# Kernel tuning notes

Hardware: AMD Instinct MI355X
Metric: run time of the kernel (lower is better)

Reference implementation:

```python
import jax, jax.numpy as jnp
import numpy as np

H = W = 2048
P = 50000  # number of peaks
BACKGROUND = 0.1


def setup_inputs() -> dict:
    key = jax.random.key(0)
    k1, k2, k3, k4 = jax.random.split(key, 4)
    # coordinate meshes, X varies along columns, Y along rows (as in np.meshgrid)
    X, Y = jnp.meshgrid(jnp.arange(W, dtype=jnp.float32), jnp.arange(H, dtype=jnp.float32))
    margin = 32.0
    pos_x = jax.random.uniform(k1, (P,), jnp.float32, margin, W - margin - 1)
    pos_y = jax.random.uniform(k2, (P,), jnp.float32, margin, H - margin - 1)
    height = jax.random.uniform(k3, (P,), jnp.float32, 0.5, 2.0)
    width = jax.random.uniform(k4, (P,), jnp.float32, 2.0, 4.0)
    return {"X": X, "Y": Y, "pos_x": pos_x, "pos_y": pos_y, "height": height, "width": width}


def _gaussian(x, y, pos_x, pos_y, height, width):
    # isotropic Gaussian peak (concrete model_fn)
    r2 = (x - pos_x) ** 2 + (y - pos_y) ** 2
    return height * jnp.exp(-r2 / (2.0 * width ** 2))


def reference(X, Y, pos_x, pos_y, height, width):
    # window size from max width (static shape choice, computed concretely)
    width_max = float(jnp.max(width))
    window_size = int(5 * width_max)
    if window_size % 2 == 0:
        window_size += 1
    half = window_size // 2

    wr = jnp.arange(-half, half + 1, dtype=jnp.int32)
    window_X, window_Y = jnp.meshgrid(wr, wr)  # (ws, ws)
    window_coords = jnp.stack([window_X.ravel(), window_Y.ravel()], axis=-1)  # (ws*ws, 2) as (x, y)

    x_idx = jnp.round(pos_x - X[0, 0]).astype(jnp.int32)
    y_idx = jnp.round(pos_y - Y[0, 0]).astype(jnp.int32)
    peak_coords = jnp.stack([x_idx, y_idx], axis=-1)  # (P, 2)
    global_coords = peak_coords[:, None, :] + window_coords[None, :, :]  # (P, ws*ws, 2)

    # evaluate peak centered at 0 on the local window: (P, ws, ws)
    local_peaks = _gaussian(
        window_X[None, :, :].astype(X.dtype),
        window_Y[None, :, :].astype(X.dtype),
        0.0, 0.0,
        height[:, None, None], width[:, None, None],
    )
    local_flat = local_peaks.reshape(pos_x.shape[0], -1)  # (P, ws*ws)

    total = jnp.zeros_like(X) + BACKGROUND
    total = total.at[global_coords[:, :, 1], global_coords[:, :, 0]].add(local_flat)
    return total
```

## Files before the change

kernel.cpp:

```cpp
#include <hip/hip_runtime.h>


#define IMG_W 2048
#define IMG_H 2048
#define CELL_SHIFT 4
#define CELLS_X 128
#define NCELL (CELLS_X * CELLS_X)
#define CAP 20
#define REG 64
#define CH 32
#define CH_PAD 40
#define CANDMAX 256

typedef _Float16 half8 __attribute__((ext_vector_type(8)));
typedef float floatx4 __attribute__((ext_vector_type(4)));

__global__ void k_bin(const float* __restrict__ px, const float* __restrict__ py,
                      const float* __restrict__ ht, const float* __restrict__ wd,
                      int P, int* __restrict__ counts, unsigned int* __restrict__ wmax,
                      float4* __restrict__ bins) {
    int i = blockIdx.x * blockDim.x + threadIdx.x;
    bool live = (i < P);
    float w = live ? wd[i] : 0.0f;
    float wr = w;
    for (int m = 32; m >= 1; m >>= 1)
        wr = fmaxf(wr, __shfl_xor(wr, m));
    if ((threadIdx.x & 63) == 0)
        atomicMax(wmax, __float_as_uint(wr));
    if (!live) return;
    float cxf = rintf(px[i]);
    float cyf = rintf(py[i]);
    int cell = (((int)cyf) >> CELL_SHIFT) * CELLS_X + (((int)cxf) >> CELL_SHIFT);
    int slot = atomicAdd(&counts[cell], 1);
    if (slot < CAP)
        bins[(size_t)cell * CAP + slot] = make_float4(cxf, cyf, ht[i], -0.5f / (w * w));
}

__global__ __launch_bounds__(512) void k_render(
    const int* __restrict__ counts, const float4* __restrict__ bins,
    const unsigned int* __restrict__ wmax, float* __restrict__ out)
{
    __shared__ _Float16 Afb[2][REG * CH_PAD];
    __shared__ _Float16 Bfb[2][REG * CH_PAD];
    __shared__ float4 cand[CANDMAX];
    __shared__ int ncand_sh;

    int flat = threadIdx.x;
    int wave = flat >> 6;
    int lane = flat & 63;

    float wm = __uint_as_float(*wmax);
    int wsz = (int)(5.0 * (double)wm);
    if ((wsz & 1) == 0) wsz++;
    int half = wsz >> 1;
    float halff = (float)half;

    int RX0 = blockIdx.x * REG;
    int RY0 = blockIdx.y * REG;

    if (flat == 0) ncand_sh = 0;
    __syncthreads();

    int cx0 = max(0, (RX0 - half) >> CELL_SHIFT);
    int cx1 = min(CELLS_X - 1, (RX0 + REG - 1 + half) >> CELL_SHIFT);
    int cy0 = max(0, (RY0 - half) >> CELL_SHIFT);
    int cy1 = min(CELLS_X - 1, (RY0 + REG - 1 + half) >> CELL_SHIFT);
    int ncx = cx1 - cx0 + 1;
    int npairs = ncx * (cy1 - cy0 + 1) * CAP;
    float ncx_rcp = __builtin_amdgcn_rcpf((float)ncx);
    int rounds = (npairs + 511) / 512;

    for (int rd = 0; rd < rounds; ++rd) {
        int pr = rd * 512 + flat;
        bool ok = false;
        float4 p = make_float4(0.f, 0.f, 0.f, 0.f);
        if (pr < npairs) {
            int c = pr / CAP;
            int s = pr - c * CAP;
            int cy = (int)(((float)c + 0.5f) * ncx_rcp);
            int cx = c - cy * ncx;
            int cell = (cy0 + cy) * CELLS_X + (cx0 + cx);
            int cnt = min(counts[cell], CAP);
            if (s < cnt) {
                p = bins[(size_t)cell * CAP + s];
                int cxi = (int)p.x, cyi = (int)p.y;
                ok = (cxi + half >= RX0 && cxi - half < RX0 + REG &&
                      cyi + half >= RY0 && cyi - half < RY0 + REG);
            }
        }
        unsigned long long m = __ballot(ok);
        if (m) {
            int leader = (int)__ffsll((unsigned long long)m) - 1;
            int base = 0;
            if (lane == leader) base = atomicAdd(&ncand_sh, __popcll(m));
            base = __shfl(base, leader);
            if (ok) {
                int pos = base + __popcll(m & ((1ull << lane) - 1));
                if (pos < CANDMAX) cand[pos] = p;
            }
        }
    }
    __syncthreads();
    int nc = min(ncand_sh, CANDMAX);
    int nch = (nc + CH - 1) / CH;

    floatx4 acc0 = {0.f, 0.f, 0.f, 0.f};
    floatx4 acc1 = {0.f, 0.f, 0.f, 0.f};
    int m0 = (wave & 3) * 16,       n0 = (wave >> 2) * 16;
    int m1 = ((wave + 8) & 3) * 16, n1 = ((wave + 8) >> 2) * 16;
    int fr = lane & 15;
    int fk = (lane >> 4) * 8;

    int side = wave >> 2;
    int oct = wave & 3;
    float base0 = side ? (float)RX0 : (float)RY0;
    float dbase = base0 + (float)lane;

    for (int ci = 0; ci < nch; ++ci) {
        int b = ci & 1;
        int c0 = ci * CH + oct * 8;
        half8 hv;
        #pragma unroll
        for (int t = 0; t < 8; ++t) {
            int k = c0 + t;
            float val = 0.0f;
            if (k < nc) {
                float4 p = cand[k];
                float d = dbase - (side ? p.x : p.y);
                if (fabsf(d) <= halff) {
                    val = __expf(p.w * d * d);
                    if (side) val *= p.z;
                }
            }
            hv[t] = (_Float16)val;
        }
        _Float16* dst = side ? &Bfb[b][lane * CH_PAD + oct * 8]
                             : &Afb[b][lane * CH_PAD + oct * 8];
        *(half8*)dst = hv;
        __syncthreads();
        half8 a0 = *(const half8*)&Afb[b][(m0 + fr) * CH_PAD + fk];
        half8 b0 = *(const half8*)&Bfb[b][(n0 + fr) * CH_PAD + fk];
        acc0 = __builtin_amdgcn_mfma_f32_16x16x32_f16(a0, b0, acc0, 0, 0, 0);
        half8 a1 = *(const half8*)&Afb[b][(m1 + fr) * CH_PAD + fk];
        half8 b1 = *(const half8*)&Bfb[b][(n1 + fr) * CH_PAD + fk];
        acc1 = __builtin_amdgcn_mfma_f32_16x16x32_f16(a1, b1, acc1, 0, 0, 0);
    }

    int col = lane & 15;
    int qr = (lane >> 4) * 4;
    {
        size_t gx = (size_t)(RX0 + n0 + col);
        size_t gy = (size_t)(RY0 + m0 + qr);
        for (int r = 0; r < 4; ++r)
            out[(gy + r) * IMG_W + gx] = acc0[r] + 0.1f;
    }
    {
        size_t gx = (size_t)(RX0 + n1 + col);
        size_t gy = (size_t)(RY0 + m1 + qr);
        for (int r = 0; r < 4; ++r)
            out[(gy + r) * IMG_W + gx] = acc1[r] + 0.1f;
    }
}

extern "C" void kernel_launch(void* const* d_in, const int* in_sizes, int n_in,
                              void* d_out, int out_size, void* d_ws, size_t ws_size,
                              hipStream_t stream) {
    const float* pos_x  = (const float*)d_in[2];
    const float* pos_y  = (const float*)d_in[3];
    const float* height = (const float*)d_in[4];
    const float* width  = (const float*)d_in[5];
    int P = in_sizes[2];
    float* out = (float*)d_out;
    char* ws = (char*)d_ws;

    unsigned int* wmax = (unsigned int*)ws;
    int* counts = (int*)(ws + 16);
    size_t bins_off = 16 + sizeof(int) * (size_t)NCELL;
    float4* bins = (float4*)(ws + bins_off);

    hipMemsetAsync(ws, 0, bins_off, stream);
    k_bin<<<(P + 255) / 256, 256, 0, stream>>>(pos_x, pos_y, height, width, P,
                                               counts, wmax, bins);
    dim3 grid(IMG_W / REG, IMG_H / REG), block(512);
    k_render<<<grid, block, 0, stream>>>(counts, bins, wmax, out);
}
```

Baseline: 105.7 us.

## Bin peaks directly into 64x64 render regions instead of fine cells

Replaces the 16x16 cell binning, along with the per-block gather-and-filter candidate scan, with direct insertion of each peak into every 64x64 render region its window overlaps. Each render block then copies its ready-made candidate list from global memory. The memset and in-kernel atomicMax width reduction become a separate single-block prep kernel that computes the max width and clears the region counts. This adds a serial single-block launch and duplicates peaks across regions, and any region with more than 160 peaks silently drops the extras.

```diff
diff --git a/kernel.cpp b/kernel.cpp
--- a/kernel.cpp
+++ b/kernel.cpp
@@ -3,47 +3,68 @@
 
 #define IMG_W 2048
 #define IMG_H 2048
-#define CELL_SHIFT 4
-#define CELLS_X 128
-#define NCELL (CELLS_X * CELLS_X)
-#define CAP 20
 #define REG 64
+#define NREG_X (IMG_W / REG)
+#define NREG (NREG_X * NREG_X)
+#define CAPR 160
 #define CH 32
 #define CH_PAD 40
-#define CANDMAX 256
 
 typedef _Float16 half8 __attribute__((ext_vector_type(8)));
 typedef float floatx4 __attribute__((ext_vector_type(4)));
 
+__global__ __launch_bounds__(1024) void k_prep(const float* __restrict__ wd, int P,
+                                               unsigned int* __restrict__ wmax,
+                                               int* __restrict__ rcounts) {
+    __shared__ float sred[16];
+    int t = threadIdx.x;
+    float m = 0.0f;
+    for (int i = t; i < P; i += 1024) m = fmaxf(m, wd[i]);
+    for (int s = 32; s >= 1; s >>= 1) m = fmaxf(m, __shfl_xor(m, s));
+    if ((t & 63) == 0) sred[t >> 6] = m;
+    __syncthreads();
+    if (t < 16) {
+        float v = sred[t];
+        for (int s = 8; s >= 1; s >>= 1) v = fmaxf(v, __shfl_xor(v, s));
+        if (t == 0) *wmax = __float_as_uint(v);
+    }
+    if (t < NREG) rcounts[t] = 0;
+}
+
 __global__ void k_bin(const float* __restrict__ px, const float* __restrict__ py,
                       const float* __restrict__ ht, const float* __restrict__ wd,
-                      int P, int* __restrict__ counts, unsigned int* __restrict__ wmax,
-                      float4* __restrict__ bins) {
+                      int P, const unsigned int* __restrict__ wmax,
+                      int* __restrict__ rcounts, float4* __restrict__ rbins) {
     int i = blockIdx.x * blockDim.x + threadIdx.x;
-    bool live = (i < P);
-    float w = live ? wd[i] : 0.0f;
-    float wr = w;
-    for (int m = 32; m >= 1; m >>= 1)
-        wr = fmaxf(wr, __shfl_xor(wr, m));
-    if ((threadIdx.x & 63) == 0)
-        atomicMax(wmax, __float_as_uint(wr));
-    if (!live) return;
+    if (i >= P) return;
+    float wm = __uint_as_float(*wmax);
+    int wsz = (int)(5.0 * (double)wm);
+    if ((wsz & 1) == 0) wsz++;
+    int half = wsz >> 1;
+
     float cxf = rintf(px[i]);
     float cyf = rintf(py[i]);
-    int cell = (((int)cyf) >> CELL_SHIFT) * CELLS_X + (((int)cxf) >> CELL_SHIFT);
-    int slot = atomicAdd(&counts[cell], 1);
-    if (slot < CAP)
-        bins[(size_t)cell * CAP + slot] = make_float4(cxf, cyf, ht[i], -0.5f / (w * w));
+    int cxi = (int)cxf, cyi = (int)cyf;
+    float w = wd[i];
+    float4 rec = make_float4(cxf, cyf, ht[i], -0.5f / (w * w));
+
+    int rx0 = max(0, (cxi - half) >> 6), rx1 = min(NREG_X - 1, (cxi + half) >> 6);
+    int ry0 = max(0, (cyi - half) >> 6), ry1 = min(NREG_X - 1, (cyi + half) >> 6);
+    for (int ry = ry0; ry <= ry1; ++ry)
+        for (int rx = rx0; rx <= rx1; ++rx) {
+            int r = ry * NREG_X + rx;
+            int slot = atomicAdd(&rcounts[r], 1);
+            if (slot < CAPR) rbins[(size_t)r * CAPR + slot] = rec;
+        }
 }
 
 __global__ __launch_bounds__(512) void k_render(
-    const int* __restrict__ counts, const float4* __restrict__ bins,
+    const int* __restrict__ rcounts, const float4* __restrict__ rbins,
     const unsigned int* __restrict__ wmax, float* __restrict__ out)
 {
     __shared__ _Float16 Afb[2][REG * CH_PAD];
     __shared__ _Float16 Bfb[2][REG * CH_PAD];
-    __shared__ float4 cand[CANDMAX];
-    __shared__ int ncand_sh;
+    __shared__ float4 cand[CAPR];
 
     int flat = threadIdx.x;
     int wave = flat >> 6;
@@ -57,51 +78,11 @@
 
     int RX0 = blockIdx.x * REG;
     int RY0 = blockIdx.y * REG;
+    int region = blockIdx.y * NREG_X + blockIdx.x;
 
-    if (flat == 0) ncand_sh = 0;
+    int nc = min(rcounts[region], CAPR);
+    if (flat < nc) cand[flat] = rbins[(size_t)region * CAPR + flat];
     __syncthreads();
-
-    int cx0 = max(0, (RX0 - half) >> CELL_SHIFT);
-    int cx1 = min(CELLS_X - 1, (RX0 + REG - 1 + half) >> CELL_SHIFT);
-    int cy0 = max(0, (RY0 - half) >> CELL_SHIFT);
-    int cy1 = min(CELLS_X - 1, (RY0 + REG - 1 + half) >> CELL_SHIFT);
-    int ncx = cx1 - cx0 + 1;
-    int npairs = ncx * (cy1 - cy0 + 1) * CAP;
-    float ncx_rcp = __builtin_amdgcn_rcpf((float)ncx);
-    int rounds = (npairs + 511) / 512;
-
-    for (int rd = 0; rd < rounds; ++rd) {
-        int pr = rd * 512 + flat;
-        bool ok = false;
-        float4 p = make_float4(0.f, 0.f, 0.f, 0.f);
-        if (pr < npairs) {
-            int c = pr / CAP;
-            int s = pr - c * CAP;
-            int cy = (int)(((float)c + 0.5f) * ncx_rcp);
-            int cx = c - cy * ncx;
-            int cell = (cy0 + cy) * CELLS_X + (cx0 + cx);
-            int cnt = min(counts[cell], CAP);
-            if (s < cnt) {
-                p = bins[(size_t)cell * CAP + s];
-                int cxi = (int)p.x, cyi = (int)p.y;
-                ok = (cxi + half >= RX0 && cxi - half < RX0 + REG &&
-                      cyi + half >= RY0 && cyi - half < RY0 + REG);
-            }
-        }
-        unsigned long long m = __ballot(ok);
-        if (m) {
-            int leader = (int)__ffsll((unsigned long long)m) - 1;
-            int base = 0;
-            if (lane == leader) base = atomicAdd(&ncand_sh, __popcll(m));
-            base = __shfl(base, leader);
-            if (ok) {
-                int pos = base + __popcll(m & ((1ull << lane) - 1));
-                if (pos < CANDMAX) cand[pos] = p;
-            }
-        }
-    }
-    __syncthreads();
-    int nc = min(ncand_sh, CANDMAX);
     int nch = (nc + CH - 1) / CH;
 
     floatx4 acc0 = {0.f, 0.f, 0.f, 0.f};
@@ -113,8 +94,7 @@
 
     int side = wave >> 2;
     int oct = wave & 3;
-    float base0 = side ? (float)RX0 : (float)RY0;
-    float dbase = base0 + (float)lane;
+    float dbase = (side ? (float)RX0 : (float)RY0) + (float)lane;
 
     for (int ci = 0; ci < nch; ++ci) {
         int b = ci & 1;
@@ -174,13 +154,13 @@
     char* ws = (char*)d_ws;
 
     unsigned int* wmax = (unsigned int*)ws;
-    int* counts = (int*)(ws + 16);
-    size_t bins_off = 16 + sizeof(int) * (size_t)NCELL;
-    float4* bins = (float4*)(ws + bins_off);
+    int* rcounts = (int*)(ws + 16);
+    size_t rbins_off = (16 + sizeof(int) * (size_t)NREG + 15) & ~(size_t)15;
+    float4* rbins = (float4*)(ws + rbins_off);
 
-    hipMemsetAsync(ws, 0, bins_off, stream);
+    k_prep<<<1, 1024, 0, stream>>>(width, P, wmax, rcounts);
     k_bin<<<(P + 255) / 256, 256, 0, stream>>>(pos_x, pos_y, height, width, P,
-                                               counts, wmax, bins);
-    dim3 grid(IMG_W / REG, IMG_H / REG), block(512);
-    k_render<<<grid, block, 0, stream>>>(counts, bins, wmax, out);
+                                               wmax, rcounts, rbins);
+    dim3 grid(NREG_X, NREG_X), block(512);
+    k_render<<<grid, block, 0, stream>>>(rcounts, rbins, wmax, out);
 }
```

Measured after the change: 123.4 us. +16.7%, slower.
